# Kernel optimization log

Measured on AMD Instinct MI355X. Metric: run time of the kernel, lower is better.

The kernel has to match this reference:

```python
import jax, jax.numpy as jnp
import numpy as np

N_NODES = 50000
NEG_SLOPE = 0.2


def _gat_conv(x, edge_index, W, att_src, att_dst, bias, heads, out_ch, concat):
    """PyG-style GATConv (add_self_loops=True, negative_slope=0.2).
    x: [N, F_in], edge_index: [2, E] (row=src, row=dst), W: [F_in, heads*out_ch],
    att_src/att_dst: [heads, out_ch], bias: [heads*out_ch] or [out_ch]."""
    N = x.shape[0]
    # add self-loops
    loops = jnp.arange(N, dtype=edge_index.dtype)
    src = jnp.concatenate([edge_index[0], loops])
    dst = jnp.concatenate([edge_index[1], loops])

    h = (x @ W).reshape(N, heads, out_ch)                 # [N, H, C]
    a_src = jnp.einsum('nhc,hc->nh', h, att_src)          # [N, H]
    a_dst = jnp.einsum('nhc,hc->nh', h, att_dst)          # [N, H]

    e = a_src[src] + a_dst[dst]                           # [E', H]
    e = jnp.where(e >= 0, e, NEG_SLOPE * e)               # leaky_relu

    # segment softmax over incoming edges of each dst node
    e_max = jax.ops.segment_max(e, dst, num_segments=N)   # [N, H]
    e_max = jnp.where(jnp.isfinite(e_max), e_max, 0.0)
    ex = jnp.exp(e - e_max[dst])                          # [E', H]
    denom = jax.ops.segment_sum(ex, dst, num_segments=N)  # [N, H]
    alpha = ex / (denom[dst] + 1e-16)                     # [E', H]

    msg = alpha[:, :, None] * h[src]                      # [E', H, C]
    out = jax.ops.segment_sum(msg, dst, num_segments=N)   # [N, H, C]

    if concat:
        out = out.reshape(N, heads * out_ch)
    else:
        out = out.mean(axis=1)
    return out + bias


def setup_inputs() -> dict:
    key = jax.random.key(0)
    ks = jax.random.split(key, 12)
    F_in, hid, H1, C, H2 = 512, 8, 8, 40, 1
    x = jax.random.normal(ks[0], (N_NODES, F_in), dtype=jnp.float32)
    edge_index = jax.random.randint(ks[1], (2, 1600000), 0, N_NODES, dtype=jnp.int64)
    s1 = 1.0 / np.sqrt(F_in)
    s2 = 1.0 / np.sqrt(hid * H1)
    return {
        'x': x,
        'edge_index': edge_index,
        'W1': jax.random.normal(ks[2], (F_in, H1 * hid), dtype=jnp.float32) * s1,
        'att_src1': jax.random.normal(ks[3], (H1, hid), dtype=jnp.float32) * s2,
        'att_dst1': jax.random.normal(ks[4], (H1, hid), dtype=jnp.float32) * s2,
        'b1': jnp.zeros((H1 * hid,), dtype=jnp.float32),
        'W2': jax.random.normal(ks[5], (H1 * hid, H2 * C), dtype=jnp.float32) * s2,
        'att_src2': jax.random.normal(ks[6], (H2, C), dtype=jnp.float32) * 0.15,
        'att_dst2': jax.random.normal(ks[7], (H2, C), dtype=jnp.float32) * 0.15,
        'b2': jnp.zeros((C,), dtype=jnp.float32),
    }


def reference(x, edge_index, W1, att_src1, att_dst1, b1, W2, att_src2, att_dst2, b2):
    # eval mode: dropout is identity
    h = _gat_conv(x, edge_index, W1, att_src1, att_dst1, b1, heads=8, out_ch=8, concat=True)
    h = jax.nn.relu(h)
    h = _gat_conv(h, edge_index, W2, att_src2, att_dst2, b2, heads=1, out_ch=40, concat=False)
    return jax.nn.log_softmax(h, axis=1)
```

## Files before the change

kernel.cpp:

```cpp
#include <hip/hip_runtime.h>
#include <math.h>

#define NNODES 50000
#define NEG_SLOPE 0.2f
#define NB 391
#define BW 128
#define CHUNK 4096
#define CAP 8128

typedef __bf16 bf16x8 __attribute__((ext_vector_type(8)));
typedef float f32x4 __attribute__((ext_vector_type(4)));

__device__ inline float rlane(float v, int l) {
    return __uint_as_float(__builtin_amdgcn_readlane((int)__float_as_uint(v), l));
}

__global__ void prep(const float* __restrict__ W1, __bf16* __restrict__ W1b,
                     int* __restrict__ bcur) {
    int i = blockIdx.x * 256 + threadIdx.x;
    if (i < NB) bcur[i] = i * CAP;
    else if (i == NB) bcur[NB] = 0;
    if (i >= 512 * 64) return;
    int k = i >> 6, n = i & 63;
    W1b[((size_t)(k >> 3) * 64 + n) * 8 + (k & 7)] = (__bf16)W1[i];
}

__global__ __launch_bounds__(256) void bin_scatter(const int* __restrict__ ei,
                                                   int E, int N, int* bcur,
                                                   int* __restrict__ tmp) {
    __shared__ int lcnt[NB];
    __shared__ int lbase[NB];
    int tid = threadIdx.x;
    int base0 = blockIdx.x * CHUNK;
    int lim = min(base0 + CHUNK, E + N);
    for (int i = tid; i < NB; i += 256) lcnt[i] = 0;
    __syncthreads();
    for (int e = base0 + tid; e < lim; e += 256) {
        int d = (e < E) ? ei[E + e] : e - E;
        atomicAdd(&lcnt[d >> 7], 1);
    }
    __syncthreads();
    for (int b = tid; b < NB; b += 256) {
        int c = lcnt[b];
        lbase[b] = c ? atomicAdd(&bcur[b], c) : 0;
    }
    __syncthreads();
    for (int i = tid; i < NB; i += 256) lcnt[i] = 0;
    __syncthreads();
    for (int e = base0 + tid; e < lim; e += 256) {
        int s, d;
        if (e < E) { s = ei[e]; d = ei[E + e]; }
        else       { s = d = e - E; }
        int b = d >> 7;
        int p = atomicAdd(&lcnt[b], 1);
        tmp[lbase[b] + p] = ((d & 127) << 16) | s;
    }
}

__global__ __launch_bounds__(256) void csr_finalize(int* __restrict__ bcur,
                                                    const int* __restrict__ tmp,
                                                    int N, int* __restrict__ off,
                                                    int* __restrict__ off_end,
                                                    int* __restrict__ slot) {
    __shared__ int cnt[BW];
    __shared__ int cur[BW];
    __shared__ int cbase_s;
    int b = blockIdx.x, tid = threadIdx.x;
    int base = b * CAP;
    int m = bcur[b] - base;
    if (tid < BW) cnt[tid] = 0;
    __syncthreads();
    for (int i = tid; i < m; i += 256)
        atomicAdd(&cnt[(tmp[base + i] >> 16) & 127], 1);
    __syncthreads();
    if (tid == 0) cbase_s = atomicAdd(&bcur[NB], m);
    int myv = (tid < BW) ? cnt[tid] : 0;
    for (int o = 1; o < BW; o <<= 1) {
        int u = 0;
        if (tid >= o && tid < BW) u = cnt[tid - o];
        __syncthreads();
        if (tid < BW) cnt[tid] += u;
        __syncthreads();
    }
    if (tid < BW) {
        int ex = cbase_s + cnt[tid] - myv;
        cur[tid] = ex;
        int g = b * BW + tid;
        if (g < N) { off[g] = ex; off_end[g] = ex + myv; }
    }
    __syncthreads();
    for (int i = tid; i < m; i += 256) {
        int v = tmp[base + i];
        int k = (v >> 16) & 127;
        int p = atomicAdd(&cur[k], 1);
        slot[p] = v & 0xFFFF;
    }
}

__global__ __launch_bounds__(256) void gemm1_mfma(const float* __restrict__ X,
                                                  const __bf16* __restrict__ W1b,
                                                  const float* __restrict__ att_s1,
                                                  const float* __restrict__ att_d1,
                                                  __bf16* __restrict__ H1b,
                                                  float* __restrict__ a_s1,
                                                  float* __restrict__ a_d1,
                                                  int M) {
    __shared__ __bf16 As[2048];
    __shared__ __bf16 Bs[2048];
    int tid = threadIdx.x, wid = tid >> 6, lane = tid & 63;
    int quad = lane >> 4, l15 = lane & 15;
    int m0 = blockIdx.x * 64;
    f32x4 acc[4] = {{0.f, 0.f, 0.f, 0.f}, {0.f, 0.f, 0.f, 0.f},
                    {0.f, 0.f, 0.f, 0.f}, {0.f, 0.f, 0.f, 0.f}};
    int mrow = tid >> 2;
    int kq_w = tid & 3;
    int xrow = min(m0 + mrow, M - 1);
    const float* xp = X + (size_t)xrow * 512 + kq_w * 8;
    for (int kb = 0; kb < 16; ++kb) {
        float4 xa = *(const float4*)(xp + kb * 32);
        float4 xb = *(const float4*)(xp + kb * 32 + 4);
        bf16x8 av;
        av[0] = (__bf16)xa.x; av[1] = (__bf16)xa.y;
        av[2] = (__bf16)xa.z; av[3] = (__bf16)xa.w;
        av[4] = (__bf16)xb.x; av[5] = (__bf16)xb.y;
        av[6] = (__bf16)xb.z; av[7] = (__bf16)xb.w;
        *(bf16x8*)(As + ((size_t)kq_w * 64 + mrow) * 8) = av;
        *(bf16x8*)(Bs + ((size_t)wid * 64 + lane) * 8) =
            *(const bf16x8*)(W1b + ((size_t)(kb * 4 + wid) * 64 + lane) * 8);
        __syncthreads();
        bf16x8 af = *(const bf16x8*)(As + ((size_t)quad * 64 + 16 * wid + l15) * 8);
#pragma unroll
        for (int t = 0; t < 4; ++t) {
            bf16x8 bf = *(const bf16x8*)(Bs + ((size_t)quad * 64 + 16 * t + l15) * 8);
            acc[t] = __builtin_amdgcn_mfma_f32_16x16x32_bf16(af, bf, acc[t], 0, 0, 0);
        }
        __syncthreads();
    }
    float asv[4], adv[4];
#pragma unroll
    for (int t = 0; t < 4; ++t) {
        asv[t] = att_s1[16 * t + l15];
        adv[t] = att_d1[16 * t + l15];
    }
#pragma unroll
    for (int t = 0; t < 4; ++t) {
#pragma unroll
        for (int r = 0; r < 4; ++r) {
            int gm = m0 + 16 * wid + quad * 4 + r;
            if (gm < M) H1b[(size_t)gm * 64 + 16 * t + l15] = (__bf16)acc[t][r];
            float ps = acc[t][r] * asv[t];
            float pd = acc[t][r] * adv[t];
            ps += __shfl_xor(ps, 1); ps += __shfl_xor(ps, 2); ps += __shfl_xor(ps, 4);
            pd += __shfl_xor(pd, 1); pd += __shfl_xor(pd, 2); pd += __shfl_xor(pd, 4);
            if (gm < M && (l15 & 7) == 0) {
                int hh = 2 * t + (l15 >> 3);
                a_s1[(size_t)gm * 8 + hh] = ps;
                a_d1[(size_t)gm * 8 + hh] = pd;
            }
        }
    }
}

__global__ __launch_bounds__(256) void agg1_fused(const int* __restrict__ off,
                                                  const int* __restrict__ off_end,
                                                  const int* __restrict__ slot,
                                                  const __bf16* __restrict__ H1b,
                                                  const float* __restrict__ a_src,
                                                  const float* __restrict__ a_dst,
                                                  const float* __restrict__ b1,
                                                  const float* __restrict__ W2,
                                                  const float* __restrict__ att_src2,
                                                  const float* __restrict__ att_dst2,
                                                  __bf16* __restrict__ H2b,
                                                  float* __restrict__ a_s2,
                                                  float* __restrict__ a_d2) {
    __shared__ float W2s[64 * 40];
    int tid = threadIdx.x;
    int wid = tid >> 6, lane = tid & 63;
    for (int i = tid; i < 64 * 40; i += 256) W2s[i] = W2[i];
    __syncthreads();
    int d = blockIdx.x * 4 + wid;
    int beg = off[d], end = off_end[d];
    int es = lane >> 3;
    int eh = lane & 7;
    float adst_c = a_dst[(size_t)d * 8 + eh];
    const __bf16* hbase = H1b + eh * 8;
    float acc[8] = {0.f, 0.f, 0.f, 0.f, 0.f, 0.f, 0.f, 0.f};
    float den_l = 0.f;
#pragma unroll 2
    for (int i = beg; i < end; i += 8) {
        int j = i + es;
        int jj = (j < end) ? j : (end - 1);
        int s = slot[jj];
        float e = a_src[(size_t)s * 8 + eh] + adst_c;
        e = (e >= 0.f) ? e : NEG_SLOPE * e;
        float w = (j < end) ? __expf(e) : 0.f;
        den_l += w;
        bf16x8 hv = *(const bf16x8*)(hbase + (size_t)s * 64);
#pragma unroll
        for (int q = 0; q < 8; ++q) acc[q] += w * (float)hv[q];
    }
#pragma unroll
    for (int m = 8; m <= 32; m <<= 1) {
        den_l += __shfl_xor(den_l, m);
#pragma unroll
        for (int q = 0; q < 8; ++q) acc[q] += __shfl_xor(acc[q], m);
    }
    float rden = 1.f / (den_l + 1e-16f);
    float vr[8];
#pragma unroll
    for (int q = 0; q < 8; ++q) {
        float t = acc[q] * rden + b1[eh * 8 + q];
        vr[q] = (t > 0.f) ? t : 0.f;
    }
    int c = lane, cc = (c < 40) ? c : 0;
    float acc2a = 0.f, acc2b = 0.f;
#pragma unroll
    for (int k = 0; k < 64; k += 2) {
        float r0 = rlane(vr[k & 7], k >> 3);
        float r1 = rlane(vr[(k + 1) & 7], (k + 1) >> 3);
        acc2a += r0 * W2s[k * 40 + cc];
        acc2b += r1 * W2s[(k + 1) * 40 + cc];
    }
    float acc2 = acc2a + acc2b;
    H2b[(size_t)d * 64 + c] = (__bf16)((c < 40) ? acc2 : 0.f);
    float ps = (c < 40) ? acc2 * att_src2[cc] : 0.f;
    float pd = (c < 40) ? acc2 * att_dst2[cc] : 0.f;
#pragma unroll
    for (int mm = 32; mm >= 1; mm >>= 1) {
        ps += __shfl_xor(ps, mm);
        pd += __shfl_xor(pd, mm);
    }
    if (lane == 0) { a_s2[d] = ps; a_d2[d] = pd; }
}

__global__ __launch_bounds__(256) void agg2(const int* __restrict__ off,
                                            const int* __restrict__ off_end,
                                            const int* __restrict__ slot,
                                            const __bf16* __restrict__ H2b,
                                            const float* __restrict__ a_src2,
                                            const float* __restrict__ a_d2,
                                            const float* __restrict__ b2,
                                            float* __restrict__ out) {
    int tid = threadIdx.x;
    int wid = tid >> 6, lane = tid & 63;
    int d = blockIdx.x * 4 + wid;
    int beg = off[d], end = off_end[d];
    int es = lane >> 3;
    int sl = lane & 7;
    float adst = a_d2[d];
    const __bf16* hbase = H2b + sl * 8;
    bool valid = (sl < 5);
    float acc[8] = {0.f, 0.f, 0.f, 0.f, 0.f, 0.f, 0.f, 0.f};
    float den_l = 0.f;
#pragma unroll 2
    for (int i = beg; i < end; i += 8) {
        int j = i + es;
        int jj = (j < end) ? j : (end - 1);
        int s = slot[jj];
        float e = a_src2[s] + adst;
        e = (e >= 0.f) ? e : NEG_SLOPE * e;
        float w = (j < end) ? __expf(e) : 0.f;
        den_l += w;
        bf16x8 hv = *(const bf16x8*)(hbase + (size_t)s * 64);
#pragma unroll
        for (int q = 0; q < 8; ++q) acc[q] += w * (float)hv[q];
    }
#pragma unroll
    for (int m = 8; m <= 32; m <<= 1) {
        den_l += __shfl_xor(den_l, m);
#pragma unroll
        for (int q = 0; q < 8; ++q) acc[q] += __shfl_xor(acc[q], m);
    }
    float rden = 1.f / (den_l + 1e-16f);
    float v[8];
    float vm = -3.0e38f;
#pragma unroll
    for (int q = 0; q < 8; ++q) {
        v[q] = acc[q] * rden + b2[valid ? sl * 8 + q : 0];
        vm = fmaxf(vm, v[q]);
    }
    if (!valid) vm = -3.0e38f;
#pragma unroll
    for (int m = 1; m <= 4; m <<= 1) vm = fmaxf(vm, __shfl_xor(vm, m));
    float se = 0.f;
#pragma unroll
    for (int q = 0; q < 8; ++q) se += __expf(v[q] - vm);
    if (!valid) se = 0.f;
#pragma unroll
    for (int m = 1; m <= 4; m <<= 1) se += __shfl_xor(se, m);
    float lse = vm + __logf(se);
    if (es == 0 && valid) {
        f32x4 o0 = {v[0] - lse, v[1] - lse, v[2] - lse, v[3] - lse};
        f32x4 o1 = {v[4] - lse, v[5] - lse, v[6] - lse, v[7] - lse};
        *(f32x4*)(out + (size_t)d * 40 + sl * 8) = o0;
        *(f32x4*)(out + (size_t)d * 40 + sl * 8 + 4) = o1;
    }
}

extern "C" void kernel_launch(void* const* d_in, const int* in_sizes, int n_in,
                              void* d_out, int out_size, void* d_ws, size_t ws_size,
                              hipStream_t stream) {
    const float* x   = (const float*)d_in[0];
    const int*   ei  = (const int*)d_in[1];
    const float* W1  = (const float*)d_in[2];
    const float* as1 = (const float*)d_in[3];
    const float* ad1 = (const float*)d_in[4];
    const float* b1  = (const float*)d_in[5];
    const float* W2  = (const float*)d_in[6];
    const float* as2 = (const float*)d_in[7];
    const float* ad2 = (const float*)d_in[8];
    const float* b2  = (const float*)d_in[9];
    float* out = (float*)d_out;

    const int N = NNODES;
    const int E = in_sizes[1] / 2;
    const int total = E + N;

    char* ws = (char*)d_ws;
    size_t o = 0;
    auto alloc = [&](size_t bytes) -> void* {
        void* p = ws + o;
        o = (o + bytes + 255) & ~(size_t)255;
        return p;
    };
    int* bcur    = (int*)alloc((size_t)(NB + 1) * 4);
    int* off     = (int*)alloc((size_t)N * 4);
    int* off_end = (int*)alloc((size_t)N * 4);
    int* slot    = (int*)alloc((size_t)total * 4);
    int* tmp     = (int*)alloc((size_t)NB * CAP * 4);
    __bf16* W1b = (__bf16*)alloc((size_t)512 * 64 * 2);
    __bf16* H1b = (__bf16*)alloc((size_t)N * 64 * 2);
    float* a_s1 = (float*)alloc((size_t)N * 8 * 4);
    float* a_d1 = (float*)alloc((size_t)N * 8 * 4);
    __bf16* H2b = (__bf16*)alloc((size_t)N * 64 * 2);
    float* a_s2 = (float*)alloc((size_t)N * 4);
    float* a_d2 = (float*)alloc((size_t)N * 4);
    (void)ws_size; (void)n_in; (void)out_size;

    prep<<<(512 * 64 + 255) / 256, 256, 0, stream>>>(W1, W1b, bcur);
    bin_scatter<<<(total + CHUNK - 1) / CHUNK, 256, 0, stream>>>(ei, E, N, bcur, tmp);
    csr_finalize<<<NB, 256, 0, stream>>>(bcur, tmp, N, off, off_end, slot);

    gemm1_mfma<<<(N + 63) / 64, 256, 0, stream>>>(x, W1b, as1, ad1, H1b, a_s1, a_d1, N);

    agg1_fused<<<N / 4, 256, 0, stream>>>(off, off_end, slot, H1b, a_s1, a_d1, b1,
                                          W2, as2, ad2, H2b, a_s2, a_d2);

    agg2<<<N / 4, 256, 0, stream>>>(off, off_end, slot, H2b, a_s2, a_d2, b2, out);
}
```

Baseline: 352.2 us.

## Batch first 64 neighbor gathers and pack layer-2 source score into H2 padding

Both aggregation kernels now load up to 64 neighbor slot indices in one coalesced read, broadcast them with shuffles, and issue all eight gather groups up front. The aim is more memory-level parallelism than the old serial loop gave; a tail loop still handles nodes with degree above 64. Layer 2's per-node source attention score is stored as an fp32 split across two padding bf16 lanes of H2, so agg2 gets it from the same row load and drops the separate a_src2 gather. The change also sets launch-bounds occupancy hints, moves the barrier after the gather phase, and uses nontemporal loads and stores, at the cost of more registers per thread.

```diff
diff --git a/kernel.cpp b/kernel.cpp
--- a/kernel.cpp
+++ b/kernel.cpp
@@ -10,6 +10,7 @@
 
 typedef __bf16 bf16x8 __attribute__((ext_vector_type(8)));
 typedef float f32x4 __attribute__((ext_vector_type(4)));
+typedef int i32x4 __attribute__((ext_vector_type(4)));
 
 __device__ inline float rlane(float v, int l) {
     return __uint_as_float(__builtin_amdgcn_readlane((int)__float_as_uint(v), l));
@@ -161,7 +162,7 @@
     }
 }
 
-__global__ __launch_bounds__(256) void agg1_fused(const int* __restrict__ off,
+__global__ __launch_bounds__(256, 6) void agg1_fused(const int* __restrict__ off,
                                                   const int* __restrict__ off_end,
                                                   const int* __restrict__ slot,
                                                   const __bf16* __restrict__ H1b,
@@ -172,23 +173,48 @@
                                                   const float* __restrict__ att_src2,
                                                   const float* __restrict__ att_dst2,
                                                   __bf16* __restrict__ H2b,
-                                                  float* __restrict__ a_s2,
                                                   float* __restrict__ a_d2) {
     __shared__ float W2s[64 * 40];
     int tid = threadIdx.x;
     int wid = tid >> 6, lane = tid & 63;
     for (int i = tid; i < 64 * 40; i += 256) W2s[i] = W2[i];
-    __syncthreads();
     int d = blockIdx.x * 4 + wid;
     int beg = off[d], end = off_end[d];
+    int deg = end - beg, dm1 = deg - 1;
     int es = lane >> 3;
     int eh = lane & 7;
     float adst_c = a_dst[(size_t)d * 8 + eh];
     const __bf16* hbase = H1b + eh * 8;
+    int sv = slot[beg + ((lane < deg) ? lane : dm1)];
+    int sg[8];
+#pragma unroll
+    for (int g = 0; g < 8; ++g) {
+        int idx = g * 8 + es;
+        sg[g] = __shfl(sv, (idx < deg) ? idx : dm1);
+    }
+    float av[8];
+#pragma unroll
+    for (int g = 0; g < 8; ++g) av[g] = a_src[(size_t)sg[g] * 8 + eh];
+    bf16x8 h[8];
+#pragma unroll
+    for (int g = 0; g < 8; ++g) h[g] = *(const bf16x8*)(hbase + (size_t)sg[g] * 64);
+    float wv[8];
+    float den_l = 0.f;
+#pragma unroll
+    for (int g = 0; g < 8; ++g) {
+        float e = av[g] + adst_c;
+        e = (e >= 0.f) ? e : NEG_SLOPE * e;
+        float w = (g * 8 + es < deg) ? __expf(e) : 0.f;
+        wv[g] = w;
+        den_l += w;
+    }
     float acc[8] = {0.f, 0.f, 0.f, 0.f, 0.f, 0.f, 0.f, 0.f};
-    float den_l = 0.f;
-#pragma unroll 2
-    for (int i = beg; i < end; i += 8) {
+#pragma unroll
+    for (int g = 0; g < 8; ++g) {
+#pragma unroll
+        for (int q = 0; q < 8; ++q) acc[q] += wv[g] * (float)h[g][q];
+    }
+    for (int i = beg + 64; i < end; i += 8) {
         int j = i + es;
         int jj = (j < end) ? j : (end - 1);
         int s = slot[jj];
@@ -213,6 +239,7 @@
         float t = acc[q] * rden + b1[eh * 8 + q];
         vr[q] = (t > 0.f) ? t : 0.f;
     }
+    __syncthreads();
     int c = lane, cc = (c < 40) ? c : 0;
     float acc2a = 0.f, acc2b = 0.f;
 #pragma unroll
@@ -223,7 +250,6 @@
         acc2b += r1 * W2s[(k + 1) * 40 + cc];
     }
     float acc2 = acc2a + acc2b;
-    H2b[(size_t)d * 64 + c] = (__bf16)((c < 40) ? acc2 : 0.f);
     float ps = (c < 40) ? acc2 * att_src2[cc] : 0.f;
     float pd = (c < 40) ? acc2 * att_dst2[cc] : 0.f;
 #pragma unroll
@@ -231,14 +257,20 @@
         ps += __shfl_xor(ps, mm);
         pd += __shfl_xor(pd, mm);
     }
-    if (lane == 0) { a_s2[d] = ps; a_d2[d] = pd; }
-}
-
-__global__ __launch_bounds__(256) void agg2(const int* __restrict__ off,
+    unsigned int pbits = __float_as_uint(ps);
+    unsigned short st;
+    if (c < 40)       st = __builtin_bit_cast(unsigned short, (__bf16)acc2);
+    else if (c == 40) st = (unsigned short)(pbits & 0xFFFF);
+    else if (c == 41) st = (unsigned short)(pbits >> 16);
+    else              st = 0;
+    ((unsigned short*)H2b)[(size_t)d * 64 + c] = st;
+    if (lane == 0) a_d2[d] = pd;
+}
+
+__global__ __launch_bounds__(256, 6) void agg2(const int* __restrict__ off,
                                             const int* __restrict__ off_end,
                                             const int* __restrict__ slot,
                                             const __bf16* __restrict__ H2b,
-                                            const float* __restrict__ a_src2,
                                             const float* __restrict__ a_d2,
                                             const float* __restrict__ b2,
                                             float* __restrict__ out) {
@@ -246,23 +278,51 @@
     int wid = tid >> 6, lane = tid & 63;
     int d = blockIdx.x * 4 + wid;
     int beg = off[d], end = off_end[d];
+    int deg = end - beg, dm1 = deg - 1;
     int es = lane >> 3;
     int sl = lane & 7;
+    int asl = (lane & 56) | 5;
     float adst = a_d2[d];
     const __bf16* hbase = H2b + sl * 8;
     bool valid = (sl < 5);
+    int sv = __builtin_nontemporal_load(slot + beg + ((lane < deg) ? lane : dm1));
+    int sg[8];
+#pragma unroll
+    for (int g = 0; g < 8; ++g) {
+        int idx = g * 8 + es;
+        sg[g] = __shfl(sv, (idx < deg) ? idx : dm1);
+    }
+    i32x4 rv[8];
+#pragma unroll
+    for (int g = 0; g < 8; ++g)
+        rv[g] = *(const i32x4*)(hbase + (size_t)sg[g] * 64);
+    float wv[8];
+    float den_l = 0.f;
+#pragma unroll
+    for (int g = 0; g < 8; ++g) {
+        float e = __uint_as_float(__shfl(rv[g][0], asl)) + adst;
+        e = (e >= 0.f) ? e : NEG_SLOPE * e;
+        float w = (g * 8 + es < deg) ? __expf(e) : 0.f;
+        wv[g] = w;
+        den_l += w;
+    }
     float acc[8] = {0.f, 0.f, 0.f, 0.f, 0.f, 0.f, 0.f, 0.f};
-    float den_l = 0.f;
-#pragma unroll 2
-    for (int i = beg; i < end; i += 8) {
+#pragma unroll
+    for (int g = 0; g < 8; ++g) {
+        bf16x8 hv = __builtin_bit_cast(bf16x8, rv[g]);
+#pragma unroll
+        for (int q = 0; q < 8; ++q) acc[q] += wv[g] * (float)hv[q];
+    }
+    for (int i = beg + 64; i < end; i += 8) {
         int j = i + es;
         int jj = (j < end) ? j : (end - 1);
         int s = slot[jj];
-        float e = a_src2[s] + adst;
+        i32x4 rvt = *(const i32x4*)(hbase + (size_t)s * 64);
+        bf16x8 hv = __builtin_bit_cast(bf16x8, rvt);
+        float e = __uint_as_float(__shfl(rvt[0], asl)) + adst;
         e = (e >= 0.f) ? e : NEG_SLOPE * e;
         float w = (j < end) ? __expf(e) : 0.f;
         den_l += w;
-        bf16x8 hv = *(const bf16x8*)(hbase + (size_t)s * 64);
 #pragma unroll
         for (int q = 0; q < 8; ++q) acc[q] += w * (float)hv[q];
     }
@@ -293,8 +353,8 @@
     if (es == 0 && valid) {
         f32x4 o0 = {v[0] - lse, v[1] - lse, v[2] - lse, v[3] - lse};
         f32x4 o1 = {v[4] - lse, v[5] - lse, v[6] - lse, v[7] - lse};
-        *(f32x4*)(out + (size_t)d * 40 + sl * 8) = o0;
-        *(f32x4*)(out + (size_t)d * 40 + sl * 8 + 4) = o1;
+        __builtin_nontemporal_store(o0, (f32x4*)(out + (size_t)d * 40 + sl * 8));
+        __builtin_nontemporal_store(o1, (f32x4*)(out + (size_t)d * 40 + sl * 8 + 4));
     }
 }
 
@@ -334,7 +394,6 @@
     float* a_s1 = (float*)alloc((size_t)N * 8 * 4);
     float* a_d1 = (float*)alloc((size_t)N * 8 * 4);
     __bf16* H2b = (__bf16*)alloc((size_t)N * 64 * 2);
-    float* a_s2 = (float*)alloc((size_t)N * 4);
     float* a_d2 = (float*)alloc((size_t)N * 4);
     (void)ws_size; (void)n_in; (void)out_size;
 
@@ -345,7 +404,7 @@
     gemm1_mfma<<<(N + 63) / 64, 256, 0, stream>>>(x, W1b, as1, ad1, H1b, a_s1, a_d1, N);
 
     agg1_fused<<<N / 4, 256, 0, stream>>>(off, off_end, slot, H1b, a_s1, a_d1, b1,
-                                          W2, as2, ad2, H2b, a_s2, a_d2);
-
-    agg2<<<N / 4, 256, 0, stream>>>(off, off_end, slot, H2b, a_s2, a_d2, b2, out);
-}
+                                          W2, as2, ad2, H2b, a_d2);
+
+    agg2<<<N / 4, 256, 0, stream>>>(off, off_end, slot, H2b, a_d2, b2, out);
+}
```

Measured after the change: 354.5 us. No clear change (+0.6%).
